# Optimization experiments

Measured on AMD Instinct MI355X. Metric: run time of the kernel, lower is better.

Reference implementation:

```python
import jax, jax.numpy as jnp
import numpy as np

S, B, H = 1024, 2, 1024
NH, NKV, HD = 16, 4, 64
E, TOPK, F = 8, 2, 2048
EPS = 1e-5


def _layer_norm(x, w, b):
    mu = jnp.mean(x, axis=-1, keepdims=True)
    var = jnp.mean(jnp.square(x - mu), axis=-1, keepdims=True)
    return (x - mu) * jax.lax.rsqrt(var + EPS) * w + b


def setup_inputs() -> dict:
    key = jax.random.key(0)
    ks = jax.random.split(key, 8)
    return {
        "hidden_states": jax.random.normal(ks[0], (S, B, H), jnp.float32),
        "ln1_weight": jnp.ones((H,), jnp.float32),
        "ln1_bias": jnp.zeros((H,), jnp.float32),
        "ln2_weight": jnp.ones((H,), jnp.float32),
        "ln2_bias": jnp.zeros((H,), jnp.float32),
        "qkv_weight": jax.random.normal(ks[1], ((NH + 2 * NKV) * HD, H), jnp.float32) * 0.02,
        "proj_weight": jax.random.normal(ks[2], (H, H), jnp.float32) * 0.02,
        "router_weight": jax.random.normal(ks[3], (E, H), jnp.float32) * 0.02,
        "moe_w1": jax.random.normal(ks[4], (E, H, F), jnp.float32) * 0.02,
        "moe_w2": jax.random.normal(ks[5], (E, F, H), jnp.float32) * 0.02,
    }


def reference(hidden_states, ln1_weight, ln1_bias, ln2_weight, ln2_bias,
              qkv_weight, proj_weight, router_weight, moe_w1, moe_w2):
    dtype = hidden_states.dtype
    # LN1 -> QKV projection
    ln1_out = _layer_norm(hidden_states, ln1_weight, ln1_bias)            # [S,B,H]
    qkv = jnp.einsum('sbh,oh->sbo', ln1_out, qkv_weight)                  # [S,B,(NH+2NKV)*HD]
    q = qkv[..., : NH * HD].reshape(S, B, NH, HD)
    k = qkv[..., NH * HD: (NH + NKV) * HD].reshape(S, B, NKV, HD)
    v = qkv[..., (NH + NKV) * HD:].reshape(S, B, NKV, HD)
    # GQA: expand kv heads (repeat_interleave along head dim)
    ratio = NH // NKV
    k = jnp.repeat(k, ratio, axis=2)                                      # [S,B,NH,HD]
    v = jnp.repeat(v, ratio, axis=2)
    # [S,B,h,d] -> [B,h,S,d]
    qb = jnp.transpose(q, (1, 2, 0, 3))
    kb = jnp.transpose(k, (1, 2, 0, 3))
    vb = jnp.transpose(v, (1, 2, 0, 3))
    scale = 1.0 / np.sqrt(HD)
    scores = jnp.einsum('bhqd,bhkd->bhqk', qb, kb) * scale                # [B,NH,S,S]
    causal = jnp.tril(jnp.ones((S, S), bool))
    scores = jnp.where(causal, scores, jnp.finfo(dtype).min)
    attn = jax.nn.softmax(scores, axis=-1)
    attn_out = jnp.einsum('bhqk,bhkd->bhqd', attn, vb)                    # [B,NH,S,HD]
    attn_out = jnp.transpose(attn_out, (2, 0, 1, 3)).reshape(S, B, H)     # [S,B,H]
    proj_out = jnp.einsum('sbh,oh->sbo', attn_out, proj_weight)
    hidden_after_attn = hidden_states + proj_out
    # LN2 -> MoE
    ln2_flat = _layer_norm(hidden_after_attn, ln2_weight, ln2_bias).reshape(-1, H)  # [T,H]
    logits = jnp.einsum('th,eh->te', ln2_flat, router_weight)             # [T,E]
    probs = jax.nn.softmax(logits, axis=-1)
    top_probs, top_idx = jax.lax.top_k(probs, TOPK)                       # [T,K]
    # combine gate: sum_k prob_k * onehot(expert_k)  -> [T,E]
    gate = jnp.sum(jax.nn.one_hot(top_idx, E, dtype=dtype) * top_probs[..., None], axis=1)
    # dense all-expert grouped GEMM equivalent of dispatch/FC1/act/FC2/combine
    h1 = jnp.einsum('th,ehf->tef', ln2_flat, moe_w1)                      # [T,E,F]
    a1 = jax.nn.gelu(h1)
    y = jnp.einsum('tef,efh->teh', a1, moe_w2)                            # [T,E,H]
    moe_out = jnp.einsum('te,teh->th', gate, y).reshape(S, B, H)
    return hidden_after_attn + moe_out
```

## Files before the change

### kernel.cpp

```cpp
#include <hip/hip_runtime.h>
#include <hip/hip_bf16.h>

typedef unsigned short u16;
typedef __attribute__((ext_vector_type(8))) short s16x8;
typedef __attribute__((ext_vector_type(4))) short s16x4;
typedef __attribute__((ext_vector_type(4))) float f32x4;

#define SEQ 1024
#define BATCH 2
#define HID 1024
#define NHEAD 16
#define NKVH 4
#define HDIM 64
#define NEXP 8
#define FFN 2048
#define TOK (SEQ*BATCH)
#define QKVO ((NHEAD + 2*NKVH)*HDIM)
#define NPART 80
#define PREC 2112

#define GL16(gp, lp) __builtin_amdgcn_global_load_lds( \
    (const __attribute__((address_space(1))) unsigned int*)(gp), \
    (__attribute__((address_space(3))) unsigned int*)(lp), 16, 0, 0)

__device__ __forceinline__ float b2f(u16 u) {
    unsigned int x = ((unsigned int)u) << 16;
    return __uint_as_float(x);
}
__device__ __forceinline__ u16 f2b(float f) {
    unsigned int x = __float_as_uint(f);
    x = (x + 0x7FFFu + ((x >> 16) & 1u)) >> 16;
    return (u16)x;
}
__device__ __forceinline__ void split2(float x, u16& hi, u16& lo) {
    hi = f2b(x);
    lo = f2b(x - b2f(hi));
}
__device__ __forceinline__ f32x4 mfma16(s16x8 a, s16x8 b, f32x4 c) {
    return __builtin_amdgcn_mfma_f32_16x16x32_bf16(a, b, c, 0, 0, 0);
}
__device__ __forceinline__ float gelu_t(float x) {
    float x3 = x * x * x;
    return 0.5f * x * (1.0f + tanhf(0.7978845608028654f * (x + 0.044715f * x3)));
}

template<int OUTMODE>
__global__ __launch_bounds__(256) void ln_k(const float* __restrict__ xin,
    const float* __restrict__ wgt, const float* __restrict__ bia,
    float* __restrict__ outf, u16* __restrict__ outh, u16* __restrict__ outl)
{
    __shared__ float red[8];
    const int t = blockIdx.x, tid = threadIdx.x;
    f32x4 u = *((const f32x4*)(xin + (size_t)t * HID) + tid);
    float s = u[0] + u[1] + u[2] + u[3];
    #pragma unroll
    for (int off = 32; off >= 1; off >>= 1) s += __shfl_xor(s, off);
    if ((tid & 63) == 0) red[tid >> 6] = s;
    __syncthreads();
    float mu = (red[0] + red[1] + red[2] + red[3]) * (1.0f / HID);
    float d0 = u[0]-mu, d1 = u[1]-mu, d2 = u[2]-mu, d3 = u[3]-mu;
    float ss = d0*d0 + d1*d1 + d2*d2 + d3*d3;
    #pragma unroll
    for (int off = 32; off >= 1; off >>= 1) ss += __shfl_xor(ss, off);
    if ((tid & 63) == 0) red[4 + (tid >> 6)] = ss;
    __syncthreads();
    float var = (red[4] + red[5] + red[6] + red[7]) * (1.0f / HID);
    float rs = 1.0f / sqrtf(var + 1e-5f);
    f32x4 wv = *((const f32x4*)wgt + tid);
    f32x4 bv = *((const f32x4*)bia + tid);
    f32x4 o;
    o[0] = d0*rs*wv[0] + bv[0];
    o[1] = d1*rs*wv[1] + bv[1];
    o[2] = d2*rs*wv[2] + bv[2];
    o[3] = d3*rs*wv[3] + bv[3];
    if (OUTMODE == 0 || OUTMODE >= 3)
        *((f32x4*)(outf + (size_t)t * HID) + tid) = o;
    if (OUTMODE == 2 || OUTMODE == 3) {
        s16x4 h, l;
        #pragma unroll
        for (int j = 0; j < 4; ++j) {
            u16 hb, lb; split2(o[j], hb, lb);
            h[j] = (short)hb; l[j] = (short)lb;
        }
        *((s16x4*)(outh + (size_t)t * HID) + tid) = h;
        *((s16x4*)(outl + (size_t)t * HID) + tid) = l;
    }
    if (OUTMODE == 4) {
        s16x4 h;
        #pragma unroll
        for (int j = 0; j < 4; ++j) h[j] = (short)f2b(o[j]);
        *((s16x4*)(outh + (size_t)t * HID) + tid) = h;
    }
}

__global__ __launch_bounds__(256) void split_cast_k(const float* __restrict__ in,
    u16* __restrict__ hi, u16* __restrict__ lo)
{
    int i = blockIdx.x * 256 + threadIdx.x;
    f32x4 v = ((const f32x4*)in)[i];
    s16x4 h, l;
    #pragma unroll
    for (int j = 0; j < 4; ++j) {
        u16 hb, lb; split2(v[j], hb, lb);
        h[j] = (short)hb; l[j] = (short)lb;
    }
    ((s16x4*)hi)[i] = h;
    ((s16x4*)lo)[i] = l;
}

__global__ __launch_bounds__(256) void trans_cast_k(const float* __restrict__ in,
    u16* __restrict__ out, int R, int C)
{
    __shared__ float tile[64][65];
    const int e = blockIdx.z;
    const float* src = in + (size_t)e * R * C;
    u16* dst = out + (size_t)e * C * R;
    const int r0 = blockIdx.y * 64, c0 = blockIdx.x * 64;
    const int tr = threadIdx.x >> 2, tc = (threadIdx.x & 3) * 16;
    #pragma unroll
    for (int j = 0; j < 4; ++j) {
        f32x4 v = *(const f32x4*)(src + (size_t)(r0 + tr) * C + c0 + tc + j * 4);
        *(f32x4*)&tile[tr][tc + j * 4] = v;
    }
    __syncthreads();
    s16x8 o0, o1;
    #pragma unroll
    for (int j = 0; j < 8; ++j) o0[j] = (short)f2b(tile[tc + j][tr]);
    #pragma unroll
    for (int j = 0; j < 8; ++j) o1[j] = (short)f2b(tile[tc + 8 + j][tr]);
    u16* dp = dst + (size_t)(c0 + tr) * R + r0 + tc;
    *(s16x8*)dp = o0;
    *(s16x8*)(dp + 8) = o1;
}

template<int AMODE, int TERMS, int EPI, int TILE, int KU>
__global__ __launch_bounds__(256, 2) void gemm_db(
    const u16* __restrict__ Ah, const u16* __restrict__ Al,
    const u16* __restrict__ Bh, const u16* __restrict__ Bl,
    void* __restrict__ Cv, const float* __restrict__ RES, float* __restrict__ C2,
    const int* __restrict__ glist, const int* __restrict__ offs,
    const int* __restrict__ cnts, const float* __restrict__ slot_p,
    int M, int N, int K, int lda, int ldb, int ldc, long long bStrideE)
{
    constexpr int BM = (TILE == 2) ? 64 : 128;
    constexpr int BN = (TILE == 0) ? 128 : 64;
    constexpr int MI = (TILE == 0) ? 4 : ((TILE == 1) ? 2 : 1);
    constexpr bool A2 = (BM == 128);
    constexpr bool B2 = (BN == 128);
    __shared__ u16 AHs[2][KU][BM][32];
    __shared__ u16 ALs[(TERMS >= 2) ? 2 : 1][(TERMS >= 2) ? KU : 1][(TERMS >= 2) ? BM : 1][32];
    __shared__ u16 BHs[2][KU][BN][32];
    __shared__ u16 BLs[(TERMS >= 3) ? 2 : 1][(TERMS >= 3) ? KU : 1][(TERMS >= 3) ? BN : 1][32];

    const int tid = threadIdx.x;
    const int m0 = blockIdx.y * BM;
    const int n0 = blockIdx.x * BN;
    int off = 0, cnt = M;
    if (AMODE != 0) {
        const int e = blockIdx.z;
        off = offs[e]; cnt = cnts[e];
        if (m0 >= cnt) return;
        long long be = (long long)e * bStrideE;
        Bh += be;
        if (TERMS >= 3) Bl += be;
    }
    const int lane = tid & 63, w = tid >> 6;
    const int wmB = (TILE == 0) ? ((w >> 1) * 64) : (w * (BM / 4));
    const int wnB = (TILE == 0) ? ((w & 1) * 64) : 0;
    const int l16 = lane & 15, grp = lane >> 4;
    const int srow = lane >> 2, schk = (lane & 3) * 8;
    const int lrA = w * (BM / 4);
    const int lrB = w * (BN / 4);

    long long ga0, ga1 = 0;
    {
        int am0 = m0 + lrA + srow;
        int am1 = am0 + 16;
        long long r0, r1;
        if (AMODE == 0) { r0 = am0; r1 = am1; }
        else if (AMODE == 1) {
            r0 = glist[off + ((am0 < cnt) ? am0 : 0)];
            r1 = A2 ? glist[off + ((am1 < cnt) ? am1 : 0)] : 0;
        } else {
            r0 = off + ((am0 < cnt) ? am0 : 0);
            r1 = A2 ? (off + ((am1 < cnt) ? am1 : 0)) : 0;
        }
        ga0 = r0 * lda + schk;
        if (A2) ga1 = r1 * lda + schk;
    }
    const long long gb0 = (long long)(n0 + lrB + srow) * ldb + schk;
    const long long gb1 = gb0 + 16LL * ldb;

    auto stage = [&](int bf, int k0) {
        #pragma unroll
        for (int u = 0; u < KU; ++u) {
            const int ko = k0 + u * 32;
            GL16(Ah + ga0 + ko, &AHs[bf][u][lrA][0]);
            if constexpr (A2) GL16(Ah + ga1 + ko, &AHs[bf][u][lrA + 16][0]);
            if constexpr (TERMS >= 2) {
                GL16(Al + ga0 + ko, &ALs[bf][u][lrA][0]);
                if constexpr (A2) GL16(Al + ga1 + ko, &ALs[bf][u][lrA + 16][0]);
            }
            GL16(Bh + gb0 + ko, &BHs[bf][u][lrB][0]);
            if constexpr (B2) GL16(Bh + gb1 + ko, &BHs[bf][u][lrB + 16][0]);
            if constexpr (TERMS >= 3) {
                GL16(Bl + gb0 + ko, &BLs[bf][u][lrB][0]);
                if constexpr (B2) GL16(Bl + gb1 + ko, &BLs[bf][u][lrB + 16][0]);
            }
        }
    };

    f32x4 acc[MI][4];
    #pragma unroll
    for (int i = 0; i < MI; ++i)
        #pragma unroll
        for (int j = 0; j < 4; ++j) acc[i][j] = f32x4{0.f, 0.f, 0.f, 0.f};

    const int nk = K / (32 * KU);
    int cur = 0;
    stage(0, 0);
    __syncthreads();
    for (int t = 0; t < nk; ++t) {
        if (t + 1 < nk) stage(cur ^ 1, (t + 1) * 32 * KU);
        #pragma unroll
        for (int u = 0; u < KU; ++u) {
            s16x8 ah[MI], al[MI], bh[4], bl[4];
            #pragma unroll
            for (int i = 0; i < MI; ++i)
                ah[i] = *(const s16x8*)&AHs[cur][u][wmB + i * 16 + l16][grp * 8];
            if constexpr (TERMS >= 2) {
                #pragma unroll
                for (int i = 0; i < MI; ++i)
                    al[i] = *(const s16x8*)&ALs[cur][u][wmB + i * 16 + l16][grp * 8];
            }
            #pragma unroll
            for (int j = 0; j < 4; ++j)
                bh[j] = *(const s16x8*)&BHs[cur][u][wnB + j * 16 + l16][grp * 8];
            if constexpr (TERMS >= 3) {
                #pragma unroll
                for (int j = 0; j < 4; ++j)
                    bl[j] = *(const s16x8*)&BLs[cur][u][wnB + j * 16 + l16][grp * 8];
            }
            #pragma unroll
            for (int i = 0; i < MI; ++i) {
                #pragma unroll
                for (int j = 0; j < 4; ++j) {
                    acc[i][j] = mfma16(ah[i], bh[j], acc[i][j]);
                    if constexpr (TERMS >= 3) acc[i][j] = mfma16(ah[i], bl[j], acc[i][j]);
                    if constexpr (TERMS >= 2) acc[i][j] = mfma16(al[i], bh[j], acc[i][j]);
                }
            }
        }
        __syncthreads();
        cur ^= 1;
    }
    #pragma unroll
    for (int i = 0; i < MI; ++i) {
        #pragma unroll
        for (int j = 0; j < 4; ++j) {
            int col = n0 + wnB + j * 16 + l16;
            #pragma unroll
            for (int r = 0; r < 4; ++r) {
                int mr = m0 + wmB + i * 16 + grp * 4 + r;
                if (AMODE != 0 && mr >= cnt) continue;
                long long crow = (AMODE == 0) ? mr : (off + mr);
                float val = acc[i][j][r];
                if (EPI == 0) {
                    ((float*)Cv)[crow * ldc + col] = val;
                } else if (EPI == 1) {
                    ((float*)Cv)[crow * ldc + col] = val + RES[crow * ldc + col];
                } else if (EPI == 2) {
                    ((u16*)Cv)[crow * ldc + col] = f2b(gelu_t(val));
                } else if (EPI == 5) {
                    ((u16*)Cv)[crow * ldc + col] = f2b(val);
                } else {
                    float v2 = val + RES[crow * ldc + col];
                    ((float*)Cv)[crow * ldc + col] = v2;
                    C2[crow * ldc + col] = v2;
                }
            }
        }
    }
}

__global__ __launch_bounds__(256) void kvprep(const float* __restrict__ qkvf,
    u16* __restrict__ kTh, u16* __restrict__ kTl,
    u16* __restrict__ vTh, u16* __restrict__ vTl)
{
    __shared__ float tile[64][68];
    const int st = blockIdx.x * 64;
    const int b = blockIdx.y & 1, kvh = blockIdx.y >> 1;
    const int tid = threadIdx.x;
    #pragma unroll
    for (int h = 0; h < 4; ++h) {
        int c = tid + h * 256;
        int srow = c >> 4, dseg = c & 15;
        f32x4 v = *(const f32x4*)(qkvf + (size_t)((st + srow) * BATCH + b) * QKVO
                                  + (NHEAD + NKVH) * HDIM + kvh * HDIM + dseg * 4);
        *(f32x4*)&tile[srow][dseg * 4] = v;
    }
    {
        int row = tid >> 2, qseg = tid & 3;
        const float* kr = qkvf + (size_t)((st + row) * BATCH + b) * QKVO
                          + NHEAD * HDIM + kvh * HDIM + qseg * 16;
        size_t ko = ((size_t)((b * NKVH + kvh) * SEQ + st + row)) * HDIM + qseg * 16;
        #pragma unroll
        for (int c = 0; c < 4; ++c) {
            f32x4 x = *(const f32x4*)(kr + c * 4);
            s16x4 vh, vl;
            #pragma unroll
            for (int j = 0; j < 4; ++j) {
                u16 hb, lb; split2(x[j], hb, lb);
                vh[j] = (short)hb; vl[j] = (short)lb;
            }
            *(s16x4*)(kTh + ko + c * 4) = vh;
            *(s16x4*)(kTl + ko + c * 4) = vl;
        }
    }
    __syncthreads();
    #pragma unroll
    for (int h = 0; h < 2; ++h) {
        int c = tid + h * 256;
        int drow = c >> 3, sseg = c & 7;
        s16x8 vh, vl;
        #pragma unroll
        for (int j = 0; j < 8; ++j) {
            u16 hb, lb; split2(tile[sseg * 8 + j][drow], hb, lb);
            vh[j] = (short)hb; vl[j] = (short)lb;
        }
        size_t oo = ((size_t)((b * NKVH + kvh) * HDIM + drow)) * SEQ + st + sseg * 8;
        *(s16x8*)(vTh + oo) = vh;
        *(s16x8*)(vTl + oo) = vl;
    }
}

__global__ __launch_bounds__(64, 3) void attn_part(
    const float* __restrict__ qkvf,
    const u16* __restrict__ kTh, const u16* __restrict__ kTl,
    const u16* __restrict__ vTh, const u16* __restrict__ vTl,
    float* __restrict__ part)
{
    __shared__ u16 plh[32][40];
    __shared__ u16 pll[32][40];
    const int p = blockIdx.x;
    int qt, c;
    if (p < 32)      { c = 0; qt = p; }
    else if (p < 56) { c = 1; qt = p - 24; }
    else if (p < 72) { c = 2; qt = p - 40; }
    else             { c = 3; qt = p - 48; }
    const int h = blockIdx.y, b = blockIdx.z;
    const int kvh = h >> 2;
    const int lane = threadIdx.x, l16 = lane & 15, grp = lane >> 4;

    s16x8 qh[2][2], ql[2][2];
    #pragma unroll
    for (int mt = 0; mt < 2; ++mt) {
        const float* qb = qkvf + (size_t)((qt * 32 + mt * 16 + l16) * BATCH + b) * QKVO
                          + h * HDIM + grp * 8;
        #pragma unroll
        for (int ks = 0; ks < 2; ++ks) {
            f32x4 x0 = *(const f32x4*)(qb + ks * 32);
            f32x4 x1 = *(const f32x4*)(qb + ks * 32 + 4);
            #pragma unroll
            for (int j = 0; j < 4; ++j) {
                u16 hb, lb;
                split2(x0[j], hb, lb);
                qh[mt][ks][j] = (short)hb; ql[mt][ks][j] = (short)lb;
                split2(x1[j], hb, lb);
                qh[mt][ks][4 + j] = (short)hb; ql[mt][ks][4 + j] = (short)lb;
            }
        }
    }
    float mrow[2][4], lsum[2][4];
    f32x4 o[2][4];
    #pragma unroll
    for (int mt = 0; mt < 2; ++mt) {
        #pragma unroll
        for (int r = 0; r < 4; ++r) { mrow[mt][r] = -__builtin_inff(); lsum[mt][r] = 0.f; }
        #pragma unroll
        for (int db = 0; db < 4; ++db) o[mt][db] = f32x4{0.f, 0.f, 0.f, 0.f};
    }

    const size_t kvbase = (size_t)(b * NKVH + kvh) * SEQ;
    const int kv0 = c * 256;
    const int kv_hi = min(kv0 + 256, qt * 32 + 32);
    const int nt = (kv_hi - kv0 + 31) >> 5;
    for (int jb = 0; jb < nt; ++jb) {
        const int kvb = kv0 + jb * 32;
        f32x4 s[2][2];
        #pragma unroll
        for (int t2 = 0; t2 < 2; ++t2) {
            size_t kb = (kvbase + kvb + t2 * 16 + l16) * HDIM + grp * 8;
            f32x4 z0 = f32x4{0.f, 0.f, 0.f, 0.f};
            f32x4 z1 = f32x4{0.f, 0.f, 0.f, 0.f};
            #pragma unroll
            for (int ks = 0; ks < 2; ++ks) {
                s16x8 kh = *(const s16x8*)(kTh + kb + ks * 32);
                s16x8 kl = *(const s16x8*)(kTl + kb + ks * 32);
                z0 = mfma16(qh[0][ks], kh, z0);
                z0 = mfma16(qh[0][ks], kl, z0);
                z0 = mfma16(ql[0][ks], kh, z0);
                z1 = mfma16(qh[1][ks], kh, z1);
                z1 = mfma16(qh[1][ks], kl, z1);
                z1 = mfma16(ql[1][ks], kh, z1);
            }
            s[0][t2] = z0; s[1][t2] = z1;
        }
        #pragma unroll
        for (int mt = 0; mt < 2; ++mt) {
            #pragma unroll
            for (int r = 0; r < 4; ++r) {
                const int qrow = qt * 32 + mt * 16 + grp * 4 + r;
                float a0 = s[mt][0][r] * 0.125f; if (kvb + l16 > qrow) a0 = -__builtin_inff();
                float a1 = s[mt][1][r] * 0.125f; if (kvb + 16 + l16 > qrow) a1 = -__builtin_inff();
                float mx = fmaxf(a0, a1);
                #pragma unroll
                for (int t = 1; t < 16; t <<= 1) mx = fmaxf(mx, __shfl_xor(mx, t));
                float mn = fmaxf(mrow[mt][r], mx);
                float sc = __expf(mrow[mt][r] - mn);
                float p0 = __expf(a0 - mn), p1 = __expf(a1 - mn);
                float ps = p0 + p1;
                #pragma unroll
                for (int t = 1; t < 16; t <<= 1) ps += __shfl_xor(ps, t);
                lsum[mt][r] = lsum[mt][r] * sc + ps;
                mrow[mt][r] = mn;
                s[mt][0][r] = p0; s[mt][1][r] = p1;
                #pragma unroll
                for (int db = 0; db < 4; ++db) o[mt][db][r] *= sc;
            }
        }
        __syncthreads();
        #pragma unroll
        for (int mt = 0; mt < 2; ++mt) {
            #pragma unroll
            for (int t2 = 0; t2 < 2; ++t2) {
                #pragma unroll
                for (int r = 0; r < 4; ++r) {
                    u16 hb, lb; split2(s[mt][t2][r], hb, lb);
                    plh[mt * 16 + grp * 4 + r][t2 * 16 + l16] = hb;
                    pll[mt * 16 + grp * 4 + r][t2 * 16 + l16] = lb;
                }
            }
        }
        __syncthreads();
        s16x8 pah0 = *(const s16x8*)&plh[l16][grp * 8];
        s16x8 pal0 = *(const s16x8*)&pll[l16][grp * 8];
        s16x8 pah1 = *(const s16x8*)&plh[16 + l16][grp * 8];
        s16x8 pal1 = *(const s16x8*)&pll[16 + l16][grp * 8];
        #pragma unroll
        for (int db = 0; db < 4; ++db) {
            size_t vo = ((size_t)((b * NKVH + kvh) * HDIM + db * 16 + l16)) * SEQ + kvb + grp * 8;
            s16x8 vh = *(const s16x8*)(vTh + vo);
            s16x8 vl = *(const s16x8*)(vTl + vo);
            o[0][db] = mfma16(pah0, vh, o[0][db]);
            o[0][db] = mfma16(pah0, vl, o[0][db]);
            o[0][db] = mfma16(pal0, vh, o[0][db]);
            o[1][db] = mfma16(pah1, vh, o[1][db]);
            o[1][db] = mfma16(pah1, vl, o[1][db]);
            o[1][db] = mfma16(pal1, vh, o[1][db]);
        }
    }
    float* rec = part + (((size_t)(b * NHEAD + h) * NPART + p) * PREC);
    #pragma unroll
    for (int mt = 0; mt < 2; ++mt) {
        #pragma unroll
        for (int db = 0; db < 4; ++db) {
            #pragma unroll
            for (int r = 0; r < 4; ++r)
                rec[(mt * 16 + grp * 4 + r) * 64 + db * 16 + l16] = o[mt][db][r];
        }
    }
    if (l16 == 0) {
        #pragma unroll
        for (int mt = 0; mt < 2; ++mt) {
            #pragma unroll
            for (int r = 0; r < 4; ++r) {
                rec[2048 + mt * 16 + grp * 4 + r] = mrow[mt][r];
                rec[2080 + mt * 16 + grp * 4 + r] = lsum[mt][r];
            }
        }
    }
}

__global__ __launch_bounds__(256) void attn_comb(const float* __restrict__ part,
    u16* __restrict__ attn_h, u16* __restrict__ attn_l)
{
    const int qt16 = blockIdx.x, h = blockIdx.y, b = blockIdx.z;
    const int qt32 = qt16 >> 1;
    const int lrow = (qt16 & 1) * 16 + (threadIdx.x >> 4);
    const int nch = (qt32 >> 3) + 1;
    const int c4 = (threadIdx.x & 15) * 4;
    const size_t base = (size_t)(b * NHEAD + h) * NPART;
    const int pbase[4] = {0, 24, 40, 48};
    float mv[4], lv[4];
    float M = -__builtin_inff();
    #pragma unroll
    for (int c = 0; c < 4; ++c) {
        if (c < nch) {
            const float* rec = part + (base + pbase[c] + qt32) * PREC;
            mv[c] = rec[2048 + lrow];
            lv[c] = rec[2080 + lrow];
            M = fmaxf(M, mv[c]);
        }
    }
    float L = 0.f;
    f32x4 acc = f32x4{0.f, 0.f, 0.f, 0.f};
    #pragma unroll
    for (int c = 0; c < 4; ++c) {
        if (c < nch) {
            const float* rec = part + (base + pbase[c] + qt32) * PREC;
            float wgt = __expf(mv[c] - M);
            L += lv[c] * wgt;
            f32x4 ov = *(const f32x4*)(rec + lrow * 64 + c4);
            acc[0] += ov[0] * wgt; acc[1] += ov[1] * wgt;
            acc[2] += ov[2] * wgt; acc[3] += ov[3] * wgt;
        }
    }
    float inv = 1.f / L;
    const int qrow = qt32 * 32 + lrow;
    size_t oo = (size_t)(qrow * BATCH + b) * HID + h * HDIM + c4;
    #pragma unroll
    for (int j = 0; j < 4; ++j) {
        u16 hb, lb; split2(acc[j] * inv, hb, lb);
        attn_h[oo + j] = hb;
        attn_l[oo + j] = lb;
    }
}

__global__ __launch_bounds__(64) void router_k(const float* __restrict__ ln2,
    const float* __restrict__ rw, int* __restrict__ e01, float* __restrict__ p01)
{
    const int t = blockIdx.x, lane = threadIdx.x;
    const float* xr = ln2 + (size_t)t * HID + lane * 16;
    float x[16];
    #pragma unroll
    for (int c = 0; c < 4; ++c) {
        f32x4 u = *(const f32x4*)(xr + c * 4);
        #pragma unroll
        for (int j = 0; j < 4; ++j) x[c * 4 + j] = u[j];
    }
    float lg[8];
    #pragma unroll
    for (int e = 0; e < 8; ++e) {
        const float* wr = rw + (size_t)e * HID + lane * 16;
        float a = 0.f;
        #pragma unroll
        for (int c = 0; c < 4; ++c) {
            f32x4 wv = *(const f32x4*)(wr + c * 4);
            #pragma unroll
            for (int j = 0; j < 4; ++j) a += x[c * 4 + j] * wv[j];
        }
        #pragma unroll
        for (int off = 32; off >= 1; off >>= 1) a += __shfl_xor(a, off);
        lg[e] = a;
    }
    float mx = lg[0];
    #pragma unroll
    for (int e = 1; e < 8; ++e) mx = fmaxf(mx, lg[e]);
    float pe[8], ssum = 0.f;
    #pragma unroll
    for (int e = 0; e < 8; ++e) { pe[e] = expf(lg[e] - mx); ssum += pe[e]; }
    float inv = 1.f / ssum;
    int e0 = 0; float b0 = -1.f;
    #pragma unroll
    for (int e = 0; e < 8; ++e) { float p = pe[e] * inv; if (p > b0) { b0 = p; e0 = e; } }
    int e1 = -1; float b1 = -1.f;
    #pragma unroll
    for (int e = 0; e < 8; ++e) {
        if (e == e0) continue;
        float p = pe[e] * inv; if (p > b1) { b1 = p; e1 = e; }
    }
    if (lane == 0) {
        e01[2 * t] = e0; e01[2 * t + 1] = e1;
        p01[2 * t] = b0; p01[2 * t + 1] = b1;
    }
}

__global__ __launch_bounds__(64) void scatter_det(const int* __restrict__ e01,
    const float* __restrict__ p01, int* __restrict__ cnt, int* __restrict__ offs,
    int* __restrict__ tok_of, float* __restrict__ slot_p, int* __restrict__ slot_of)
{
    const int e = blockIdx.x;
    const int lane = threadIdx.x;
    int myc[8] = {0, 0, 0, 0, 0, 0, 0, 0};
    for (int i = lane; i < 2 * TOK; i += 64) {
        int ei = e01[i];
        #pragma unroll
        for (int ee = 0; ee < 8; ++ee) myc[ee] += (ei == ee) ? 1 : 0;
    }
    #pragma unroll
    for (int ee = 0; ee < 8; ++ee) {
        int v = myc[ee];
        #pragma unroll
        for (int off = 32; off >= 1; off >>= 1) v += __shfl_xor(v, off);
        myc[ee] = v;
    }
    int base = 0;
    #pragma unroll
    for (int ee = 0; ee < 8; ++ee) if (ee < e) base += myc[ee];
    if (lane == 0) { cnt[e] = myc[e]; offs[e] = base; }
    for (int c = 0; c < TOK; c += 64) {
        int t = c + lane;
        int kk = -1;
        if (e01[2 * t] == e) kk = 0;
        else if (e01[2 * t + 1] == e) kk = 1;
        int f = (kk >= 0) ? 1 : 0;
        int sc = f;
        #pragma unroll
        for (int o = 1; o < 64; o <<= 1) {
            int nn = __shfl_up(sc, o);
            if (lane >= o) sc += nn;
        }
        if (kk >= 0) {
            int slot = base + sc - 1;
            tok_of[slot] = t;
            slot_p[slot] = p01[2 * t + kk];
            slot_of[2 * t + kk] = slot;
        }
        base += __shfl(sc, 63);
    }
}

__global__ __launch_bounds__(256) void moe_comb(const u16* __restrict__ yb,
    const int* __restrict__ slot_of, const float* __restrict__ p01,
    float* __restrict__ out)
{
    const int t = blockIdx.x;
    const int c4 = threadIdx.x * 4;
    const int s0 = slot_of[2 * t], s1 = slot_of[2 * t + 1];
    const float p0 = p01[2 * t], p1 = p01[2 * t + 1];
    s16x4 y0 = *(const s16x4*)(yb + (size_t)s0 * HID + c4);
    s16x4 y1 = *(const s16x4*)(yb + (size_t)s1 * HID + c4);
    f32x4 o = *(f32x4*)(out + (size_t)t * HID + c4);
    #pragma unroll
    for (int j = 0; j < 4; ++j)
        o[j] += p0 * b2f((u16)y0[j]) + p1 * b2f((u16)y1[j]);
    *(f32x4*)(out + (size_t)t * HID + c4) = o;
}

__global__ void sentinel_k(float* out) {
    out[blockIdx.x * 256 + threadIdx.x] = 12345.0f;
}

extern "C" void kernel_launch(void* const* d_in, const int* in_sizes, int n_in,
                              void* d_out, int out_size, void* d_ws, size_t ws_size,
                              hipStream_t stream)
{
    (void)in_sizes; (void)n_in; (void)out_size;
    const float* hs    = (const float*)d_in[0];
    const float* ln1w  = (const float*)d_in[1];
    const float* ln1b  = (const float*)d_in[2];
    const float* ln2w  = (const float*)d_in[3];
    const float* ln2b  = (const float*)d_in[4];
    const float* qkvw  = (const float*)d_in[5];
    const float* projw = (const float*)d_in[6];
    const float* rw    = (const float*)d_in[7];
    const float* w1    = (const float*)d_in[8];
    const float* w2    = (const float*)d_in[9];
    float* out = (float*)d_out;
    char* ws = (char*)d_ws;

    size_t o = 0;
    auto alloc = [&](size_t bytes) -> void* {
        void* p = ws + o; o += (bytes + 255) & ~(size_t)255; return p;
    };
    u16*   w1t    = (u16*)alloc((size_t)NEXP * FFN * HID * 2);
    u16*   w2t    = (u16*)alloc((size_t)NEXP * HID * FFN * 2);
    u16*   qkvwh  = (u16*)alloc((size_t)QKVO * HID * 2);
    u16*   qkvwl  = (u16*)alloc((size_t)QKVO * HID * 2);
    u16*   projwh = (u16*)alloc((size_t)HID * HID * 2);
    u16*   projwl = (u16*)alloc((size_t)HID * HID * 2);
    u16*   ln1h   = (u16*)alloc((size_t)TOK * HID * 2);
    u16*   ln1l   = (u16*)alloc((size_t)TOK * HID * 2);
    float* qkvf   = (float*)alloc((size_t)TOK * QKVO * 4);
    u16*   kTh    = (u16*)alloc((size_t)BATCH * NKVH * SEQ * HDIM * 2);
    u16*   kTl    = (u16*)alloc((size_t)BATCH * NKVH * SEQ * HDIM * 2);
    u16*   vTh    = (u16*)alloc((size_t)BATCH * NKVH * HDIM * SEQ * 2);
    u16*   vTl    = (u16*)alloc((size_t)BATCH * NKVH * HDIM * SEQ * 2);
    float* haf    = (float*)alloc((size_t)TOK * HID * 4);
    u16*   ln2h   = (u16*)alloc((size_t)TOK * HID * 2);
    u16*   a1b    = (u16*)alloc((size_t)TOK * 2 * FFN * 2);
    int*   e01    = (int*)alloc(TOK * 2 * 4);
    float* p01    = (float*)alloc(TOK * 2 * 4);
    int*   cnt    = (int*)alloc(256);
    int*   offs   = (int*)alloc(256);
    int*   tok_of = (int*)alloc(TOK * 2 * 4);
    float* slot_p = (float*)alloc(TOK * 2 * 4);
    int*   slot_of = (int*)alloc(TOK * 2 * 4);
    size_t need = o;

    if (ws_size < need) {
        sentinel_k<<<TOK * HID / 256, 256, 0, stream>>>(out);
        return;
    }

    u16* attnh = ln1h;
    u16* attnl = ln1l;
    float* ln2f = qkvf;
    u16*  yb = (u16*)qkvf;
    float* part = (float*)w1t;

    split_cast_k<<<QKVO * HID / 4 / 256, 256, 0, stream>>>(qkvw, qkvwh, qkvwl);
    split_cast_k<<<HID * HID / 4 / 256, 256, 0, stream>>>(projw, projwh, projwl);
    ln_k<2><<<TOK, 256, 0, stream>>>(hs, ln1w, ln1b, nullptr, ln1h, ln1l);
    gemm_db<0, 3, 0, 2, 1><<<dim3(QKVO / 64, TOK / 64, 1), 256, 0, stream>>>(
        ln1h, ln1l, qkvwh, qkvwl, qkvf, nullptr, nullptr, nullptr, nullptr, nullptr, nullptr,
        TOK, QKVO, HID, HID, HID, QKVO, 0);
    kvprep<<<dim3(SEQ / 64, BATCH * NKVH), 256, 0, stream>>>(qkvf, kTh, kTl, vTh, vTl);
    attn_part<<<dim3(NPART, NHEAD, BATCH), 64, 0, stream>>>(
        qkvf, kTh, kTl, vTh, vTl, part);
    attn_comb<<<dim3(SEQ / 16, NHEAD, BATCH), 256, 0, stream>>>(part, attnh, attnl);
    gemm_db<0, 3, 4, 2, 1><<<dim3(HID / 64, TOK / 64, 1), 256, 0, stream>>>(
        attnh, attnl, projwh, projwl, haf, hs, out, nullptr, nullptr, nullptr, nullptr,
        TOK, HID, HID, HID, HID, HID, 0);
    ln_k<4><<<TOK, 256, 0, stream>>>(haf, ln2w, ln2b, ln2f, ln2h, nullptr);
    trans_cast_k<<<dim3(FFN / 64, HID / 64, NEXP), 256, 0, stream>>>(w1, w1t, HID, FFN);
    trans_cast_k<<<dim3(HID / 64, FFN / 64, NEXP), 256, 0, stream>>>(w2, w2t, FFN, HID);
    router_k<<<TOK, 64, 0, stream>>>(ln2f, rw, e01, p01);
    scatter_det<<<NEXP, 64, 0, stream>>>(e01, p01, cnt, offs, tok_of, slot_p, slot_of);
    gemm_db<1, 1, 2, 1, 2><<<dim3(FFN / 64, TOK / 128, NEXP), 256, 0, stream>>>(
        ln2h, nullptr, w1t, nullptr, a1b, nullptr, nullptr, tok_of, offs, cnt, nullptr,
        0, FFN, HID, HID, HID, FFN, (long long)FFN * HID);
    gemm_db<2, 1, 5, 1, 2><<<dim3(HID / 64, TOK / 128, NEXP), 256, 0, stream>>>(
        a1b, nullptr, w2t, nullptr, yb, nullptr, nullptr, tok_of, offs, cnt, slot_p,
        0, HID, FFN, FFN, FFN, HID, (long long)HID * FFN);
    moe_comb<<<TOK, 256, 0, stream>>>(yb, slot_of, p01, out);
}
```

Before: 317.0 us.

## Remap GEMM block indices for XCD-aware L2 locality and merge split-cast launches

GEMM grids become 1D, and block IDs are remapped so that consecutive IDs, which round-robin across the 8 XCDs, are grouped by XCD. For dense GEMMs each XCD gets a contiguous range of N columns, so its weight tiles stay in its private L2. For MoE GEMMs the low 3 bits select the expert, so each XCD handles one expert's weights. Separately, the two weight split-cast launches are fused into one kernel to save a launch. The remap relies on the hardware dispatching blocks round-robin across XCDs and on nx and the expert count both being multiples of 8.

```diff
diff --git a/kernel.cpp b/kernel.cpp
--- a/kernel.cpp
+++ b/kernel.cpp
@@ -93,10 +93,14 @@
     }
 }
 
-__global__ __launch_bounds__(256) void split_cast_k(const float* __restrict__ in,
-    u16* __restrict__ hi, u16* __restrict__ lo)
+__global__ __launch_bounds__(256) void split_cast2_k(
+    const float* __restrict__ inA, u16* __restrict__ hiA, u16* __restrict__ loA, int nA4,
+    const float* __restrict__ inB, u16* __restrict__ hiB, u16* __restrict__ loB)
 {
     int i = blockIdx.x * 256 + threadIdx.x;
+    const float* in; u16* hi; u16* lo;
+    if (i < nA4) { in = inA; hi = hiA; lo = loA; }
+    else { i -= nA4; in = inB; hi = hiB; lo = loB; }
     f32x4 v = ((const f32x4*)in)[i];
     s16x4 h, l;
     #pragma unroll
@@ -140,7 +144,7 @@
     void* __restrict__ Cv, const float* __restrict__ RES, float* __restrict__ C2,
     const int* __restrict__ glist, const int* __restrict__ offs,
     const int* __restrict__ cnts, const float* __restrict__ slot_p,
-    int M, int N, int K, int lda, int ldb, int ldc, long long bStrideE)
+    int M, int N, int K, int lda, int ldb, int ldc, long long bStrideE, int nx)
 {
     constexpr int BM = (TILE == 2) ? 64 : 128;
     constexpr int BN = (TILE == 0) ? 128 : 64;
@@ -153,11 +157,18 @@
     __shared__ u16 BLs[(TERMS >= 3) ? 2 : 1][(TERMS >= 3) ? KU : 1][(TERMS >= 3) ? BN : 1][32];
 
     const int tid = threadIdx.x;
-    const int m0 = blockIdx.y * BM;
-    const int n0 = blockIdx.x * BN;
+    const int bid = blockIdx.x;
+    int m0, n0;
     int off = 0, cnt = M;
-    if (AMODE != 0) {
-        const int e = blockIdx.z;
+    if (AMODE == 0) {
+        const int xcd = bid & 7, j = bid >> 3;
+        const int npx = nx >> 3;
+        n0 = (xcd * npx + j % npx) * BN;
+        m0 = (j / npx) * BM;
+    } else {
+        const int e = bid & 7, j = bid >> 3;
+        n0 = (j % nx) * BN;
+        m0 = (j / nx) * BM;
         off = offs[e]; cnt = cnts[e];
         if (m0 >= cnt) return;
         long long be = (long long)e * bStrideE;
@@ -700,29 +711,29 @@
     u16*  yb = (u16*)qkvf;
     float* part = (float*)w1t;
 
-    split_cast_k<<<QKVO * HID / 4 / 256, 256, 0, stream>>>(qkvw, qkvwh, qkvwl);
-    split_cast_k<<<HID * HID / 4 / 256, 256, 0, stream>>>(projw, projwh, projwl);
+    split_cast2_k<<<(QKVO * HID + HID * HID) / 4 / 256, 256, 0, stream>>>(
+        qkvw, qkvwh, qkvwl, QKVO * HID / 4, projw, projwh, projwl);
     ln_k<2><<<TOK, 256, 0, stream>>>(hs, ln1w, ln1b, nullptr, ln1h, ln1l);
-    gemm_db<0, 3, 0, 2, 1><<<dim3(QKVO / 64, TOK / 64, 1), 256, 0, stream>>>(
+    gemm_db<0, 3, 0, 2, 1><<<(QKVO / 64) * (TOK / 64), 256, 0, stream>>>(
         ln1h, ln1l, qkvwh, qkvwl, qkvf, nullptr, nullptr, nullptr, nullptr, nullptr, nullptr,
-        TOK, QKVO, HID, HID, HID, QKVO, 0);
+        TOK, QKVO, HID, HID, HID, QKVO, 0, QKVO / 64);
     kvprep<<<dim3(SEQ / 64, BATCH * NKVH), 256, 0, stream>>>(qkvf, kTh, kTl, vTh, vTl);
     attn_part<<<dim3(NPART, NHEAD, BATCH), 64, 0, stream>>>(
         qkvf, kTh, kTl, vTh, vTl, part);
     attn_comb<<<dim3(SEQ / 16, NHEAD, BATCH), 256, 0, stream>>>(part, attnh, attnl);
-    gemm_db<0, 3, 4, 2, 1><<<dim3(HID / 64, TOK / 64, 1), 256, 0, stream>>>(
+    gemm_db<0, 3, 4, 2, 1><<<(HID / 64) * (TOK / 64), 256, 0, stream>>>(
         attnh, attnl, projwh, projwl, haf, hs, out, nullptr, nullptr, nullptr, nullptr,
-        TOK, HID, HID, HID, HID, HID, 0);
+        TOK, HID, HID, HID, HID, HID, 0, HID / 64);
     ln_k<4><<<TOK, 256, 0, stream>>>(haf, ln2w, ln2b, ln2f, ln2h, nullptr);
     trans_cast_k<<<dim3(FFN / 64, HID / 64, NEXP), 256, 0, stream>>>(w1, w1t, HID, FFN);
     trans_cast_k<<<dim3(HID / 64, FFN / 64, NEXP), 256, 0, stream>>>(w2, w2t, FFN, HID);
     router_k<<<TOK, 64, 0, stream>>>(ln2f, rw, e01, p01);
     scatter_det<<<NEXP, 64, 0, stream>>>(e01, p01, cnt, offs, tok_of, slot_p, slot_of);
-    gemm_db<1, 1, 2, 1, 2><<<dim3(FFN / 64, TOK / 128, NEXP), 256, 0, stream>>>(
+    gemm_db<1, 1, 2, 1, 2><<<NEXP * (FFN / 64) * (TOK / 128), 256, 0, stream>>>(
         ln2h, nullptr, w1t, nullptr, a1b, nullptr, nullptr, tok_of, offs, cnt, nullptr,
-        0, FFN, HID, HID, HID, FFN, (long long)FFN * HID);
-    gemm_db<2, 1, 5, 1, 2><<<dim3(HID / 64, TOK / 128, NEXP), 256, 0, stream>>>(
+        0, FFN, HID, HID, HID, FFN, (long long)FFN * HID, FFN / 64);
+    gemm_db<2, 1, 5, 1, 2><<<NEXP * (HID / 64) * (TOK / 128), 256, 0, stream>>>(
         a1b, nullptr, w2t, nullptr, yb, nullptr, nullptr, tok_of, offs, cnt, slot_p,
-        0, HID, FFN, FFN, FFN, HID, (long long)HID * FFN);
+        0, HID, FFN, FFN, FFN, HID, (long long)HID * FFN, HID / 64);
     moe_comb<<<TOK, 256, 0, stream>>>(yb, slot_of, p01, out);
 }
```

Measured after the change: 305.9 us. 3.5% less time.
